# Optimization experiments

Hardware: AMD Instinct MI355X
Metric: run time of the kernel (lower is better)

Reference implementation:

```python
import jax, jax.numpy as jnp
import numpy as np

B, T, I, H, O = 64, 512, 512, 1024, 1


def setup_inputs() -> dict:
    key = jax.random.key(0)
    ks = jax.random.split(key, 12)
    s_i = 1.0 / np.sqrt(H)  # torch LSTM init scale ~ U(-1/sqrt(H), 1/sqrt(H)); normal*scale is fine for a numeric baseline
    return {
        "x": jax.random.normal(ks[0], (B, T, I), dtype=jnp.float32),
        "W_ih0": jax.random.normal(ks[1], (4 * H, I), dtype=jnp.float32) * s_i,
        "W_hh0": jax.random.normal(ks[2], (4 * H, H), dtype=jnp.float32) * s_i,
        "b_ih0": jax.random.normal(ks[3], (4 * H,), dtype=jnp.float32) * s_i,
        "b_hh0": jax.random.normal(ks[4], (4 * H,), dtype=jnp.float32) * s_i,
        "W_ih1": jax.random.normal(ks[5], (4 * H, H), dtype=jnp.float32) * s_i,
        "W_hh1": jax.random.normal(ks[6], (4 * H, H), dtype=jnp.float32) * s_i,
        "b_ih1": jax.random.normal(ks[7], (4 * H,), dtype=jnp.float32) * s_i,
        "b_hh1": jax.random.normal(ks[8], (4 * H,), dtype=jnp.float32) * s_i,
        "W_out": jax.random.normal(ks[9], (O, H), dtype=jnp.float32) * s_i,
        "b_out": jax.random.normal(ks[10], (O,), dtype=jnp.float32) * s_i,
    }


def _lstm_layer(x, W_ih, W_hh, b_ih, b_hh):
    # x: [B, T, D_in] -> h_seq: [B, T, H]. Gate order (i, f, g, o) as in torch.
    h_dim = W_hh.shape[1]
    batch = x.shape[0]
    # Precompute input contribution for all timesteps: [B, T, 4H]
    gx = jnp.einsum("btd,gd->btg", x, W_ih) + b_ih + b_hh
    gx_t = jnp.swapaxes(gx, 0, 1)  # [T, B, 4H]

    def step(carry, g_in):
        h, c = carry
        gates = g_in + h @ W_hh.T  # [B, 4H]
        i, f, g, o = jnp.split(gates, 4, axis=-1)
        i = jax.nn.sigmoid(i)
        f = jax.nn.sigmoid(f)
        g = jnp.tanh(g)
        o = jax.nn.sigmoid(o)
        c = f * c + i * g
        h = o * jnp.tanh(c)
        return (h, c), h

    h0 = jnp.zeros((batch, h_dim), dtype=x.dtype)
    c0 = jnp.zeros((batch, h_dim), dtype=x.dtype)
    _, hs = jax.lax.scan(step, (h0, c0), gx_t)  # hs: [T, B, H]
    return jnp.swapaxes(hs, 0, 1)


def reference(x, W_ih0, W_hh0, b_ih0, b_hh0, W_ih1, W_hh1, b_ih1, b_hh1, W_out, b_out):
    h1 = _lstm_layer(x, W_ih0, W_hh0, b_ih0, b_hh0)   # layer 0 (dropout=0.0 between layers)
    h2 = _lstm_layer(h1, W_ih1, W_hh1, b_ih1, b_hh1)  # layer 1
    last = h2[:, -1, :]                               # [B, H]
    out = last @ W_out.T + b_out                      # [B, O]
    return jax.nn.sigmoid(out)                        # sigmoid=True
```

## Files before the change

kernel.cpp:

```cpp
#include <hip/hip_runtime.h>
#include <hip/hip_bf16.h>


namespace {

constexpr int B_ = 64, T_ = 512, I_ = 512, H_ = 1024;
constexpr int NWG = 256, NTHR = 256;
constexpr int BH = B_ * H_;

typedef __attribute__((ext_vector_type(8))) short short8;
typedef __attribute__((ext_vector_type(4))) float f32x4;

#define MFMA16(a, b, c) __builtin_amdgcn_mfma_f32_16x16x32_bf16((a), (b), (c), 0, 0, 0)

__device__ __forceinline__ float sigm(float x)  { return 1.f / (1.f + __expf(-x)); }
__device__ __forceinline__ float tanhx(float x) { return 2.f / (1.f + __expf(-2.f * x)) - 1.f; }

__device__ __forceinline__ unsigned f2bf(float f) {
  unsigned u = __float_as_uint(f);
  unsigned rnd = 0x7FFFu + ((u >> 16) & 1u);
  return (u + rnd) >> 16;
}
__device__ __forceinline__ float bf2f(unsigned short s) {
  return __uint_as_float(((unsigned)s) << 16);
}

__global__ void cvt_bf16_k(const float* __restrict__ src, unsigned short* __restrict__ dst, int n4) {
  int i = blockIdx.x * 256 + threadIdx.x;
  if (i >= n4) return;
  float4 v = reinterpret_cast<const float4*>(src)[i];
  ushort4 o;
  o.x = (unsigned short)f2bf(v.x); o.y = (unsigned short)f2bf(v.y);
  o.z = (unsigned short)f2bf(v.z); o.w = (unsigned short)f2bf(v.w);
  reinterpret_cast<ushort4*>(dst)[i] = o;
}

__global__ void zero_init_k(unsigned short* __restrict__ h1, unsigned short* __restrict__ h2,
                            unsigned* __restrict__ bar) {
  int i = blockIdx.x * 256 + threadIdx.x;
  if (i < BH) h1[(size_t)T_ * BH + i] = 0;
  if (i < BH) h2[(size_t)T_ * BH + i] = 0;
  if (i < 1024) bar[i] = 0;
}

__global__ __launch_bounds__(NTHR, 1) void lstm_fused(
    const unsigned short* __restrict__ xb,
    const unsigned short* __restrict__ wih0, const unsigned short* __restrict__ whh0,
    const float* __restrict__ bih0, const float* __restrict__ bhh0,
    const unsigned short* __restrict__ wih1, const unsigned short* __restrict__ whh1,
    const float* __restrict__ bih1, const float* __restrict__ bhh1,
    unsigned short* __restrict__ h1rec, unsigned short* __restrict__ h2rec,
    unsigned* __restrict__ bars)
{
  __shared__ unsigned short s_win[32 * 1024];
  __shared__ unsigned short s_whh[32 * 1024];

  const int tid   = threadIdx.x;
  const int wg    = blockIdx.x;
  const int layer = wg >> 7;
  const int lwg   = wg & 127;
  const int wave  = tid >> 6;
  const int lane  = tid & 63;
  const int j0    = lwg * 8;
  const int n     = lane & 15;
  const int u4    = lane >> 4;
  const int k0    = u4 * 8;
  const int arow  = wave * 16 + n;
  const int swz_n = (n & 7) << 3;

  const unsigned short* w_in = layer ? wih1 : wih0;
  const unsigned short* w_hh = layer ? whh1 : whh0;
  const float* b_i = layer ? bih1 : bih0;
  const float* b_h = layer ? bhh1 : bhh0;
  unsigned short* rec = layer ? h2rec : h1rec;
  const int K_IN = layer ? 1024 : 512;

  unsigned* grp = bars + (wg >> 3) * 32;

  const int CH_IN = K_IN / 8;
  for (int c = tid; c < 32 * CH_IN; c += NTHR) {
    int r = c / CH_IN;
    int kc = (c % CH_IN) * 8;
    int grow = (r & 3) * H_ + j0 + (r >> 2);
    *reinterpret_cast<short8*>(&s_win[r * K_IN + (kc ^ ((r & 7) << 3))]) =
        *reinterpret_cast<const short8*>(&w_in[(size_t)grow * K_IN + kc]);
  }
  for (int c = tid; c < 32 * 128; c += NTHR) {
    int r = c >> 7;
    int kc = (c & 127) * 8;
    int grow = (r & 3) * H_ + j0 + (r >> 2);
    *reinterpret_cast<short8*>(&s_whh[r * H_ + (kc ^ ((r & 7) << 3))]) =
        *reinterpret_cast<const short8*>(&w_hh[(size_t)grow * H_ + kc]);
  }
  float bias0[4], bias1[4];
  #pragma unroll
  for (int g = 0; g < 4; ++g) {
    bias0[g] = b_i[g * H_ + j0 + u4]     + b_h[g * H_ + j0 + u4];
    bias1[g] = b_i[g * H_ + j0 + 4 + u4] + b_h[g * H_ + j0 + 4 + u4];
  }
  __syncthreads();

  float cst0 = 0.f, cst1 = 0.f;
  f32x4 na0 = {0.f, 0.f, 0.f, 0.f}, na1 = {0.f, 0.f, 0.f, 0.f};

  if (layer == 0) {
    const unsigned short* a_in = xb + (size_t)arow * (T_ * I_) + k0;
    #pragma unroll
    for (int kk = 0; kk < 512 / 32; ++kk) {
      short8 bv = *reinterpret_cast<const short8*>(a_in + kk * 32);
      const int col = (k0 + kk * 32) ^ swz_n;
      na0 = MFMA16(*reinterpret_cast<const short8*>(&s_win[n * 512 + col]),        bv, na0);
      na1 = MFMA16(*reinterpret_cast<const short8*>(&s_win[(16 + n) * 512 + col]), bv, na1);
    }
  }

  for (int p = 0; p <= T_ + 1; ++p) {
    if (p > 0) {
      const unsigned tgt = (unsigned)p * 8u;
      for (;;) {
        unsigned v = 0xFFFFFFFFu;
        if (lane < 32)
          v = __hip_atomic_load(bars + lane * 32, __ATOMIC_RELAXED, __HIP_MEMORY_SCOPE_AGENT);
        if (__all((int)(lane >= 32 || v >= tgt))) break;
        __builtin_amdgcn_s_sleep(1);
      }
      __builtin_amdgcn_fence(__ATOMIC_ACQUIRE, "workgroup");
    }

    f32x4 acc0 = na0, acc1 = na1;
    const int t = layer ? p - 2 : p;

    if (t >= 0 && t < T_) {
      const unsigned short* a_h = rec + (size_t)(T_ - t) * BH + (size_t)arow * H_ + k0;
      short8 hf[32];
      #pragma unroll
      for (int kk = 0; kk < 32; ++kk)
        hf[kk] = *reinterpret_cast<const short8*>(a_h + kk * 32);
      #pragma unroll
      for (int kk = 0; kk < 32; ++kk) {
        const int col = (k0 + kk * 32) ^ swz_n;
        acc0 = MFMA16(*reinterpret_cast<const short8*>(&s_whh[n * H_ + col]),        hf[kk], acc0);
        acc1 = MFMA16(*reinterpret_cast<const short8*>(&s_whh[(16 + n) * H_ + col]), hf[kk], acc1);
      }

      float gi0 = sigm(acc0[0] + bias0[0]);
      float gf0 = sigm(acc0[1] + bias0[1]);
      float gg0 = tanhx(acc0[2] + bias0[2]);
      float go0 = sigm(acc0[3] + bias0[3]);
      cst0 = gf0 * cst0 + gi0 * gg0;
      float hv0 = go0 * tanhx(cst0);

      float gi1 = sigm(acc1[0] + bias1[0]);
      float gf1 = sigm(acc1[1] + bias1[1]);
      float gg1 = tanhx(acc1[2] + bias1[2]);
      float go1 = sigm(acc1[3] + bias1[3]);
      cst1 = gf1 * cst1 + gi1 * gg1;
      float hv1 = go1 * tanhx(cst1);

      unsigned a16 = f2bf(hv0) & 0xFFFFu;
      unsigned b16 = f2bf(hv1) & 0xFFFFu;
      unsigned a1 = __shfl(a16, (lane & 15) | 16, 64);
      unsigned a2 = __shfl(a16, (lane & 15) | 32, 64);
      unsigned a3 = __shfl(a16, (lane & 15) | 48, 64);
      unsigned b1 = __shfl(b16, (lane & 15) | 16, 64);
      unsigned b2 = __shfl(b16, (lane & 15) | 32, 64);
      unsigned b3 = __shfl(b16, (lane & 15) | 48, 64);
      if (lane < 16) {
        unsigned long long qa = (unsigned long long)(a16 | (a1 << 16)) |
                                ((unsigned long long)(a2 | (a3 << 16)) << 32);
        unsigned long long qb = (unsigned long long)(b16 | (b1 << 16)) |
                                ((unsigned long long)(b2 | (b3 << 16)) << 32);
        unsigned long long* dst = (unsigned long long*)
            (rec + (size_t)(T_ - t - 1) * BH + (size_t)(wave * 16 + lane) * H_ + j0);
        __hip_atomic_store(dst,     qa, __ATOMIC_RELAXED, __HIP_MEMORY_SCOPE_AGENT);
        __hip_atomic_store(dst + 1, qb, __ATOMIC_RELAXED, __HIP_MEMORY_SCOPE_AGENT);
      }
    }

    __syncthreads();
    if (tid == 0)
      __hip_atomic_fetch_add(grp, 1u, __ATOMIC_RELAXED, __HIP_MEMORY_SCOPE_AGENT);

    na0 = (f32x4){0.f, 0.f, 0.f, 0.f};
    na1 = (f32x4){0.f, 0.f, 0.f, 0.f};
    const int tn = layer ? p - 1 : p + 1;
    if (tn >= 0 && tn < T_) {
      if (layer == 0) {
        const unsigned short* a_in = xb + (size_t)arow * (T_ * I_) + (size_t)tn * I_ + k0;
        #pragma unroll
        for (int kk = 0; kk < 512 / 32; ++kk) {
          short8 bv = *reinterpret_cast<const short8*>(a_in + kk * 32);
          const int col = (k0 + kk * 32) ^ swz_n;
          na0 = MFMA16(*reinterpret_cast<const short8*>(&s_win[n * 512 + col]),        bv, na0);
          na1 = MFMA16(*reinterpret_cast<const short8*>(&s_win[(16 + n) * 512 + col]), bv, na1);
        }
      } else {
        const unsigned short* a_in = h1rec + (size_t)(T_ - 1 - tn) * BH + (size_t)arow * H_ + k0;
        #pragma unroll
        for (int kk = 0; kk < 1024 / 32; ++kk) {
          short8 bv = *reinterpret_cast<const short8*>(a_in + kk * 32);
          const int col = (k0 + kk * 32) ^ swz_n;
          na0 = MFMA16(*reinterpret_cast<const short8*>(&s_win[n * 1024 + col]),        bv, na0);
          na1 = MFMA16(*reinterpret_cast<const short8*>(&s_win[(16 + n) * 1024 + col]), bv, na1);
        }
      }
    }
  }
}

__global__ void out_head(const unsigned short* __restrict__ h2,
                         const float* __restrict__ W_out,
                         const float* __restrict__ b_out,
                         float* __restrict__ out) {
  int b = blockIdx.x;
  int lane = threadIdx.x;
  float s = 0.f;
  for (int k = lane; k < H_; k += 64)
    s += bf2f(h2[(size_t)b * H_ + k]) * W_out[k];
  #pragma unroll
  for (int off = 32; off; off >>= 1) s += __shfl_down(s, off, 64);
  if (lane == 0) out[b] = sigm(s + b_out[0]);
}

}

extern "C" void kernel_launch(void* const* d_in, const int* in_sizes, int n_in,
                              void* d_out, int out_size, void* d_ws, size_t ws_size,
                              hipStream_t stream) {
  const float* x    = (const float*)d_in[0];
  const float* Wih0 = (const float*)d_in[1];
  const float* Whh0 = (const float*)d_in[2];
  const float* bih0 = (const float*)d_in[3];
  const float* bhh0 = (const float*)d_in[4];
  const float* Wih1 = (const float*)d_in[5];
  const float* Whh1 = (const float*)d_in[6];
  const float* bih1 = (const float*)d_in[7];
  const float* bhh1 = (const float*)d_in[8];
  const float* Wout = (const float*)d_in[9];
  const float* bout = (const float*)d_in[10];
  float* out = (float*)d_out;

  char* ws = (char*)d_ws;
  size_t off = 0;
  auto alloc = [&](size_t bytes) -> char* {
    char* p = ws + off;
    off += (bytes + 4095) & ~(size_t)4095;
    return p;
  };
  const size_t REC = (size_t)(T_ + 1) * BH * 2;

  unsigned* bar        = (unsigned*)alloc(4096);
  unsigned short* xb   = (unsigned short*)alloc((size_t)B_ * T_ * I_ * 2);
  unsigned short* wih0 = (unsigned short*)alloc((size_t)4 * H_ * I_ * 2);
  unsigned short* whh0 = (unsigned short*)alloc((size_t)4 * H_ * H_ * 2);
  unsigned short* wih1 = (unsigned short*)alloc((size_t)4 * H_ * H_ * 2);
  unsigned short* whh1 = (unsigned short*)alloc((size_t)4 * H_ * H_ * 2);
  unsigned short* h1   = (unsigned short*)alloc(REC);
  unsigned short* h2   = (unsigned short*)alloc(REC);

  auto cvt = [&](const float* s, unsigned short* d, int nelem) {
    int n4 = nelem / 4;
    cvt_bf16_k<<<(n4 + 255) / 256, 256, 0, stream>>>(s, d, n4);
  };
  cvt(x,    xb,   B_ * T_ * I_);
  cvt(Wih0, wih0, 4 * H_ * I_);
  cvt(Whh0, whh0, 4 * H_ * H_);
  cvt(Wih1, wih1, 4 * H_ * H_);
  cvt(Whh1, whh1, 4 * H_ * H_);
  zero_init_k<<<(BH + 255) / 256, 256, 0, stream>>>(h1, h2, bar);

  lstm_fused<<<NWG, NTHR, 0, stream>>>(
      xb, wih0, whh0, bih0, bhh0, wih1, whh1, bih1, bhh1, h1, h2, bar);

  out_head<<<B_, 64, 0, stream>>>(h2, Wout, bout, out);
}
```

Baseline: 4.248 ms.

## Use hierarchical grid barrier and pre-swizzle weights into MFMA fragment order in LDS

The grid barrier changes so that only wave 0 of eight leader workgroups polls the 32 group counters. Each leader then publishes a release flag, and every other workgroup or wave spins on that single flag. This replaces 256 workgroups each polling 32 counters. Separately, the weights are stored in LDS already in per-lane MFMA operand order, so each A-fragment load is a contiguous 16-byte-per-lane read with no XOR swizzle address math. The hierarchical barrier adds an extra hop of latency per timestep in exchange for less atomic traffic contention.

```diff
diff --git a/kernel.cpp b/kernel.cpp
--- a/kernel.cpp
+++ b/kernel.cpp
@@ -40,7 +40,7 @@
   int i = blockIdx.x * 256 + threadIdx.x;
   if (i < BH) h1[(size_t)T_ * BH + i] = 0;
   if (i < BH) h2[(size_t)T_ * BH + i] = 0;
-  if (i < 1024) bar[i] = 0;
+  if (i < 2048) bar[i] = 0;
 }
 
 __global__ __launch_bounds__(NTHR, 1) void lstm_fused(
@@ -52,8 +52,8 @@
     unsigned short* __restrict__ h1rec, unsigned short* __restrict__ h2rec,
     unsigned* __restrict__ bars)
 {
-  __shared__ unsigned short s_win[32 * 1024];
-  __shared__ unsigned short s_whh[32 * 1024];
+  __shared__ unsigned short s_win[32768];
+  __shared__ unsigned short s_whh[32768];
 
   const int tid   = threadIdx.x;
   const int wg    = blockIdx.x;
@@ -66,7 +66,6 @@
   const int u4    = lane >> 4;
   const int k0    = u4 * 8;
   const int arow  = wave * 16 + n;
-  const int swz_n = (n & 7) << 3;
 
   const unsigned short* w_in = layer ? wih1 : wih0;
   const unsigned short* w_hh = layer ? whh1 : whh0;
@@ -74,23 +73,28 @@
   const float* b_h = layer ? bhh1 : bhh0;
   unsigned short* rec = layer ? h2rec : h1rec;
   const int K_IN = layer ? 1024 : 512;
+  const int NKI  = K_IN / 32;
 
   unsigned* grp = bars + (wg >> 3) * 32;
-
-  const int CH_IN = K_IN / 8;
-  for (int c = tid; c < 32 * CH_IN; c += NTHR) {
-    int r = c / CH_IN;
-    int kc = (c % CH_IN) * 8;
-    int grow = (r & 3) * H_ + j0 + (r >> 2);
-    *reinterpret_cast<short8*>(&s_win[r * K_IN + (kc ^ ((r & 7) << 3))]) =
-        *reinterpret_cast<const short8*>(&w_in[(size_t)grow * K_IN + kc]);
-  }
-  for (int c = tid; c < 32 * 128; c += NTHR) {
-    int r = c >> 7;
-    int kc = (c & 127) * 8;
-    int grow = (r & 3) * H_ + j0 + (r >> 2);
-    *reinterpret_cast<short8*>(&s_whh[r * H_ + (kc ^ ((r & 7) << 3))]) =
-        *reinterpret_cast<const short8*>(&w_hh[(size_t)grow * H_ + kc]);
+  unsigned* rel = bars + 1024 + (wg & 7) * 32;
+
+  for (int c = tid; c < 2 * NKI * 64; c += NTHR) {
+    int l  = c & 63;
+    int kk = (c >> 6) % NKI;
+    int rt = c / (NKI * 64);
+    int rr = l & 15, q = l >> 4;
+    int grow = (rr & 3) * H_ + j0 + rt * 4 + (rr >> 2);
+    *reinterpret_cast<short8*>(&s_win[c * 8]) =
+        *reinterpret_cast<const short8*>(&w_in[(size_t)grow * K_IN + kk * 32 + q * 8]);
+  }
+  for (int c = tid; c < 2 * 32 * 64; c += NTHR) {
+    int l  = c & 63;
+    int kk = (c >> 6) & 31;
+    int rt = c >> 11;
+    int rr = l & 15, q = l >> 4;
+    int grow = (rr & 3) * H_ + j0 + rt * 4 + (rr >> 2);
+    *reinterpret_cast<short8*>(&s_whh[c * 8]) =
+        *reinterpret_cast<const short8*>(&w_hh[(size_t)grow * H_ + kk * 32 + q * 8]);
   }
   float bias0[4], bias1[4];
   #pragma unroll
@@ -106,23 +110,34 @@
   if (layer == 0) {
     const unsigned short* a_in = xb + (size_t)arow * (T_ * I_) + k0;
     #pragma unroll
-    for (int kk = 0; kk < 512 / 32; ++kk) {
+    for (int kk = 0; kk < 16; ++kk) {
       short8 bv = *reinterpret_cast<const short8*>(a_in + kk * 32);
-      const int col = (k0 + kk * 32) ^ swz_n;
-      na0 = MFMA16(*reinterpret_cast<const short8*>(&s_win[n * 512 + col]),        bv, na0);
-      na1 = MFMA16(*reinterpret_cast<const short8*>(&s_win[(16 + n) * 512 + col]), bv, na1);
+      na0 = MFMA16(*reinterpret_cast<const short8*>(&s_win[(kk * 64 + lane) * 8]),          bv, na0);
+      na1 = MFMA16(*reinterpret_cast<const short8*>(&s_win[((16 + kk) * 64 + lane) * 8]),   bv, na1);
     }
   }
 
   for (int p = 0; p <= T_ + 1; ++p) {
     if (p > 0) {
       const unsigned tgt = (unsigned)p * 8u;
-      for (;;) {
-        unsigned v = 0xFFFFFFFFu;
-        if (lane < 32)
-          v = __hip_atomic_load(bars + lane * 32, __ATOMIC_RELAXED, __HIP_MEMORY_SCOPE_AGENT);
-        if (__all((int)(lane >= 32 || v >= tgt))) break;
-        __builtin_amdgcn_s_sleep(1);
+      if (wg < 8) {
+        if (wave == 0) {
+          for (;;) {
+            unsigned v = 0xFFFFFFFFu;
+            if (lane < 32)
+              v = __hip_atomic_load(bars + lane * 32, __ATOMIC_RELAXED, __HIP_MEMORY_SCOPE_AGENT);
+            if (__all((int)(lane >= 32 || v >= tgt))) break;
+            __builtin_amdgcn_s_sleep(1);
+          }
+          if (lane == 0)
+            __hip_atomic_store(rel, (unsigned)p, __ATOMIC_RELAXED, __HIP_MEMORY_SCOPE_AGENT);
+        } else {
+          while (__hip_atomic_load(rel, __ATOMIC_RELAXED, __HIP_MEMORY_SCOPE_AGENT) < (unsigned)p)
+            __builtin_amdgcn_s_sleep(1);
+        }
+      } else {
+        while (__hip_atomic_load(rel, __ATOMIC_RELAXED, __HIP_MEMORY_SCOPE_AGENT) < (unsigned)p)
+          __builtin_amdgcn_s_sleep(1);
       }
       __builtin_amdgcn_fence(__ATOMIC_ACQUIRE, "workgroup");
     }
@@ -138,9 +153,8 @@
         hf[kk] = *reinterpret_cast<const short8*>(a_h + kk * 32);
       #pragma unroll
       for (int kk = 0; kk < 32; ++kk) {
-        const int col = (k0 + kk * 32) ^ swz_n;
-        acc0 = MFMA16(*reinterpret_cast<const short8*>(&s_whh[n * H_ + col]),        hf[kk], acc0);
-        acc1 = MFMA16(*reinterpret_cast<const short8*>(&s_whh[(16 + n) * H_ + col]), hf[kk], acc1);
+        acc0 = MFMA16(*reinterpret_cast<const short8*>(&s_whh[(kk * 64 + lane) * 8]),        hf[kk], acc0);
+        acc1 = MFMA16(*reinterpret_cast<const short8*>(&s_whh[((32 + kk) * 64 + lane) * 8]), hf[kk], acc1);
       }
 
       float gi0 = sigm(acc0[0] + bias0[0]);
@@ -188,20 +202,18 @@
       if (layer == 0) {
         const unsigned short* a_in = xb + (size_t)arow * (T_ * I_) + (size_t)tn * I_ + k0;
         #pragma unroll
-        for (int kk = 0; kk < 512 / 32; ++kk) {
+        for (int kk = 0; kk < 16; ++kk) {
           short8 bv = *reinterpret_cast<const short8*>(a_in + kk * 32);
-          const int col = (k0 + kk * 32) ^ swz_n;
-          na0 = MFMA16(*reinterpret_cast<const short8*>(&s_win[n * 512 + col]),        bv, na0);
-          na1 = MFMA16(*reinterpret_cast<const short8*>(&s_win[(16 + n) * 512 + col]), bv, na1);
+          na0 = MFMA16(*reinterpret_cast<const short8*>(&s_win[(kk * 64 + lane) * 8]),        bv, na0);
+          na1 = MFMA16(*reinterpret_cast<const short8*>(&s_win[((16 + kk) * 64 + lane) * 8]), bv, na1);
         }
       } else {
         const unsigned short* a_in = h1rec + (size_t)(T_ - 1 - tn) * BH + (size_t)arow * H_ + k0;
         #pragma unroll
-        for (int kk = 0; kk < 1024 / 32; ++kk) {
+        for (int kk = 0; kk < 32; ++kk) {
           short8 bv = *reinterpret_cast<const short8*>(a_in + kk * 32);
-          const int col = (k0 + kk * 32) ^ swz_n;
-          na0 = MFMA16(*reinterpret_cast<const short8*>(&s_win[n * 1024 + col]),        bv, na0);
-          na1 = MFMA16(*reinterpret_cast<const short8*>(&s_win[(16 + n) * 1024 + col]), bv, na1);
+          na0 = MFMA16(*reinterpret_cast<const short8*>(&s_win[(kk * 64 + lane) * 8]),        bv, na0);
+          na1 = MFMA16(*reinterpret_cast<const short8*>(&s_win[((32 + kk) * 64 + lane) * 8]), bv, na1);
         }
       }
     }
@@ -249,7 +261,7 @@
   };
   const size_t REC = (size_t)(T_ + 1) * BH * 2;
 
-  unsigned* bar        = (unsigned*)alloc(4096);
+  unsigned* bar        = (unsigned*)alloc(8192);
   unsigned short* xb   = (unsigned short*)alloc((size_t)B_ * T_ * I_ * 2);
   unsigned short* wih0 = (unsigned short*)alloc((size_t)4 * H_ * I_ * 2);
   unsigned short* whh0 = (unsigned short*)alloc((size_t)4 * H_ * H_ * 2);
```

New measurement: 4.271 ms. Within noise of the previous version (+0.6%).
